# Kernel optimization log

Hardware: AMD Instinct MI355X
Metric: run time of the kernel (lower is better)

The kernel has to match this reference:

```python
import jax, jax.numpy as jnp
import numpy as np

# uniform-measure init scales from torch_model.init_embedding_scale()
MIN_MEAN = (0.0001 + 0.01) / 2.0
MIN_VAR = 0.01 - MIN_MEAN
DELTA_MEAN = (0.9 + 0.999) / 2.0
DELTA_VAR = 0.999 - DELTA_MEAN
EPS = 1e-8

B, V, D = 131072, 100000, 128


def setup_inputs() -> dict:
    key = jax.random.key(0)
    k1, k2, k3, k4 = jax.random.split(key, 4)
    return {
        "t1x": jax.random.randint(k1, (B,), 0, V),
        "t2x": jax.random.randint(k2, (B,), 0, V),
        "min_embed_table": jax.random.normal(k3, (V, D), jnp.float32),
        "delta_embed_table": jax.random.normal(k4, (V, D), jnp.float32),
    }


def _log_vol(mn, mx):
    # log volume of a box under the uniform (unit-cube) measure; [*, D] -> [*]
    return jnp.sum(jnp.log(jnp.maximum(mx - mn, EPS)), axis=-1)


def _box(idx, min_table, delta_table):
    # embedding lookup + affine rescale into the unit cube (get_word_embedding)
    mn = min_table[idx] * MIN_VAR + MIN_MEAN
    dl = delta_table[idx] * DELTA_VAR + DELTA_MEAN
    return mn, mn + dl


def reference(t1x, t2x, min_embed_table, delta_embed_table):
    t1_min, t1_max = _box(t1x, min_embed_table, delta_embed_table)  # [B, D]
    t2_min, t2_max = _box(t2x, min_embed_table, delta_embed_table)

    # unit_cube.calc_join_and_meet
    join_min = jnp.minimum(t1_min, t2_min)
    join_max = jnp.maximum(t1_max, t2_max)
    meet_min = jnp.maximum(t1_min, t2_min)
    meet_max = jnp.minimum(t1_max, t2_max)
    disjoint = jnp.any(meet_max <= meet_min, axis=-1)  # [B] bool

    t1_log = _log_vol(t1_min, t1_max)      # [B]
    t2_log = _log_vol(t2_min, t2_max)
    meet_log = _log_vol(meet_min, meet_max)
    join_log = _log_vol(join_min, join_max)

    # log P(t1 | t2) = log vol(meet) - log vol(t2)
    cond_log = meet_log - t2_log

    # positive pairs: overlap -> -log P(t1|t2); disjoint -> upper-bound surrogate
    # upper bound: P(t1, t2) <= vol(t1)*vol(t2)/vol(join)  =>  P(t1|t2) <= vol(t1)/vol(join)
    pos_overlap = -cond_log
    pos_disjoint = -(t1_log - join_log)

    # negative pairs: overlap -> -log(1 - P(t1|t2)); disjoint -> 0 loss
    neg_overlap = -jnp.log(jnp.maximum(1.0 - jnp.exp(cond_log), EPS))

    # vectorized version of the per-sample python loop over the disjoint flag
    train_pos_prob = jnp.where(disjoint, pos_disjoint, pos_overlap)  # [B]
    train_neg_prob = jnp.where(disjoint, jnp.zeros_like(neg_overlap), neg_overlap)
    return train_pos_prob, train_neg_prob
```

## Files before the change

kernel.cpp:

```cpp
#include <hip/hip_runtime.h>
#include <math.h>


#define EPSF 1e-8f

__global__ __launch_bounds__(256) void box_loss_kernel(
    const int* __restrict__ t1x, const int* __restrict__ t2x,
    const float* __restrict__ min_t, const float* __restrict__ delta_t,
    float* __restrict__ out, int B)
{
    const float MIN_MEAN   = (float)((0.0001 + 0.01) / 2.0);
    const float MIN_VAR    = (float)(0.01 - (0.0001 + 0.01) / 2.0);
    const float DELTA_MEAN = (float)((0.9 + 0.999) / 2.0);
    const float DELTA_VAR  = (float)(0.999 - (0.9 + 0.999) / 2.0);

    int gid  = blockIdx.x * blockDim.x + threadIdx.x;
    int s    = gid >> 5;
    int lane = threadIdx.x & 31;
    if (s >= B) return;

    long i1 = (long)t1x[s];
    long i2 = (long)t2x[s];

    const float4* m1 = reinterpret_cast<const float4*>(min_t   + i1 * 128);
    const float4* d1 = reinterpret_cast<const float4*>(delta_t + i1 * 128);
    const float4* m2 = reinterpret_cast<const float4*>(min_t   + i2 * 128);
    const float4* d2 = reinterpret_cast<const float4*>(delta_t + i2 * 128);

    float4 vm1 = m1[lane];
    float4 vd1 = d1[lane];
    float4 vm2 = m2[lane];
    float4 vd2 = d2[lane];

    const float* pm1 = reinterpret_cast<const float*>(&vm1);
    const float* pd1 = reinterpret_cast<const float*>(&vd1);
    const float* pm2 = reinterpret_cast<const float*>(&vm2);
    const float* pd2 = reinterpret_cast<const float*>(&vd2);

    float t1_log = 0.f, t2_log = 0.f, meet_log = 0.f, join_log = 0.f;
    int disjoint = 0;

    #pragma unroll
    for (int k = 0; k < 4; ++k) {
        float t1min = fmaf(pm1[k], MIN_VAR, MIN_MEAN);
        float t1dl  = fmaf(pd1[k], DELTA_VAR, DELTA_MEAN);
        float t1max = t1min + t1dl;

        float t2min = fmaf(pm2[k], MIN_VAR, MIN_MEAN);
        float t2dl  = fmaf(pd2[k], DELTA_VAR, DELTA_MEAN);
        float t2max = t2min + t2dl;

        float jm = fminf(t1min, t2min);
        float jM = fmaxf(t1max, t2max);
        float mm = fmaxf(t1min, t2min);
        float mM = fminf(t1max, t2max);

        disjoint |= (mM <= mm) ? 1 : 0;

        t1_log   += __logf(fmaxf(t1max - t1min, EPSF));
        t2_log   += __logf(fmaxf(t2max - t2min, EPSF));
        meet_log += __logf(fmaxf(mM - mm, EPSF));
        join_log += __logf(fmaxf(jM - jm, EPSF));
    }

    #pragma unroll
    for (int m = 16; m >= 1; m >>= 1) {
        t1_log   += __shfl_xor(t1_log,   m, 64);
        t2_log   += __shfl_xor(t2_log,   m, 64);
        meet_log += __shfl_xor(meet_log, m, 64);
        join_log += __shfl_xor(join_log, m, 64);
        disjoint |= __shfl_xor(disjoint, m, 64);
    }

    if (lane == 0) {
        float cond = meet_log - t2_log;
        float pos, neg;
        if (disjoint) {
            pos = join_log - t1_log;
            neg = 0.f;
        } else {
            pos = -cond;
            neg = -logf(fmaxf(1.f - expf(cond), EPSF));
        }
        out[s]     = pos;
        out[B + s] = neg;
    }
}

extern "C" void kernel_launch(void* const* d_in, const int* in_sizes, int n_in,
                              void* d_out, int out_size, void* d_ws, size_t ws_size,
                              hipStream_t stream) {
    const int*   t1x     = (const int*)d_in[0];
    const int*   t2x     = (const int*)d_in[1];
    const float* min_t   = (const float*)d_in[2];
    const float* delta_t = (const float*)d_in[3];
    float*       out     = (float*)d_out;

    int B = in_sizes[0];
    int threads = 256;
    int blocks  = (B * 32 + threads - 1) / threads;
    box_loss_kernel<<<blocks, threads, 0, stream>>>(t1x, t2x, min_t, delta_t, out, B);
}
```

Baseline: 141.2 us.

## Use 8 lanes per sample and replace per-element logs with products

Each sample is now handled by 8 lanes instead of 32, with every lane loading four float4 chunks per row. Per-element logarithms are replaced by running products of the widths, followed by one log per accumulator. The disjoint flag now comes from the minimum meet width. This cuts transcendental work, shuffle rounds and redundant index loads. Products of 16 widths could underflow when meet widths are near EPS (1e-8), which risks precision.

Result: faster. 137.4 us (-2.7%).

```diff
diff --git a/kernel.cpp b/kernel.cpp
--- a/kernel.cpp
+++ b/kernel.cpp
@@ -15,68 +15,81 @@
     const float DELTA_VAR  = (float)(0.999 - (0.9 + 0.999) / 2.0);
 
     int gid  = blockIdx.x * blockDim.x + threadIdx.x;
-    int s    = gid >> 5;
-    int lane = threadIdx.x & 31;
+    int s    = gid >> 3;
+    int lane = threadIdx.x & 7;
     if (s >= B) return;
 
-    long i1 = (long)t1x[s];
-    long i2 = (long)t2x[s];
+    size_t i1 = (size_t)t1x[s];
+    size_t i2 = (size_t)t2x[s];
 
     const float4* m1 = reinterpret_cast<const float4*>(min_t   + i1 * 128);
     const float4* d1 = reinterpret_cast<const float4*>(delta_t + i1 * 128);
     const float4* m2 = reinterpret_cast<const float4*>(min_t   + i2 * 128);
     const float4* d2 = reinterpret_cast<const float4*>(delta_t + i2 * 128);
 
-    float4 vm1 = m1[lane];
-    float4 vd1 = d1[lane];
-    float4 vm2 = m2[lane];
-    float4 vd2 = d2[lane];
+    float4 a1[4], b1[4], a2[4], b2[4];
+    #pragma unroll
+    for (int c = 0; c < 4; ++c) {
+        int off = c * 8 + lane;
+        a1[c] = m1[off];
+        b1[c] = d1[off];
+        a2[c] = m2[off];
+        b2[c] = d2[off];
+    }
 
-    const float* pm1 = reinterpret_cast<const float*>(&vm1);
-    const float* pd1 = reinterpret_cast<const float*>(&vd1);
-    const float* pm2 = reinterpret_cast<const float*>(&vm2);
-    const float* pd2 = reinterpret_cast<const float*>(&vd2);
-
-    float t1_log = 0.f, t2_log = 0.f, meet_log = 0.f, join_log = 0.f;
-    int disjoint = 0;
+    float p1 = 1.f, p2 = 1.f, pm = 1.f, pj = 1.f;
+    float wmin = 1e30f;
 
     #pragma unroll
-    for (int k = 0; k < 4; ++k) {
-        float t1min = fmaf(pm1[k], MIN_VAR, MIN_MEAN);
-        float t1dl  = fmaf(pd1[k], DELTA_VAR, DELTA_MEAN);
-        float t1max = t1min + t1dl;
+    for (int c = 0; c < 4; ++c) {
+        const float* pa1 = reinterpret_cast<const float*>(&a1[c]);
+        const float* pb1 = reinterpret_cast<const float*>(&b1[c]);
+        const float* pa2 = reinterpret_cast<const float*>(&a2[c]);
+        const float* pb2 = reinterpret_cast<const float*>(&b2[c]);
+        #pragma unroll
+        for (int k = 0; k < 4; ++k) {
+            float t1min = fmaf(pa1[k], MIN_VAR, MIN_MEAN);
+            float w1    = fmaf(pb1[k], DELTA_VAR, DELTA_MEAN);
+            float t2min = fmaf(pa2[k], MIN_VAR, MIN_MEAN);
+            float w2    = fmaf(pb2[k], DELTA_VAR, DELTA_MEAN);
+            float t1max = t1min + w1;
+            float t2max = t2min + w2;
 
-        float t2min = fmaf(pm2[k], MIN_VAR, MIN_MEAN);
-        float t2dl  = fmaf(pd2[k], DELTA_VAR, DELTA_MEAN);
-        float t2max = t2min + t2dl;
+            float mm_ = fmaxf(t1min, t2min);
+            float mM_ = fminf(t1max, t2max);
+            float jm_ = fminf(t1min, t2min);
+            float jM_ = fmaxf(t1max, t2max);
 
-        float jm = fminf(t1min, t2min);
-        float jM = fmaxf(t1max, t2max);
-        float mm = fmaxf(t1min, t2min);
-        float mM = fminf(t1max, t2max);
+            float wm = mM_ - mm_;
+            float wj = jM_ - jm_;
 
-        disjoint |= (mM <= mm) ? 1 : 0;
-
-        t1_log   += __logf(fmaxf(t1max - t1min, EPSF));
-        t2_log   += __logf(fmaxf(t2max - t2min, EPSF));
-        meet_log += __logf(fmaxf(mM - mm, EPSF));
-        join_log += __logf(fmaxf(jM - jm, EPSF));
+            wmin = fminf(wmin, wm);
+            p1 *= w1;
+            p2 *= w2;
+            pm *= fmaxf(wm, EPSF);
+            pj *= wj;
+        }
     }
 
+    float l1 = __logf(p1);
+    float l2 = __logf(p2);
+    float lm = __logf(pm);
+    float lj = __logf(pj);
+
     #pragma unroll
-    for (int m = 16; m >= 1; m >>= 1) {
-        t1_log   += __shfl_xor(t1_log,   m, 64);
-        t2_log   += __shfl_xor(t2_log,   m, 64);
-        meet_log += __shfl_xor(meet_log, m, 64);
-        join_log += __shfl_xor(join_log, m, 64);
-        disjoint |= __shfl_xor(disjoint, m, 64);
+    for (int m = 4; m >= 1; m >>= 1) {
+        l1   += __shfl_xor(l1,   m, 64);
+        l2   += __shfl_xor(l2,   m, 64);
+        lm   += __shfl_xor(lm,   m, 64);
+        lj   += __shfl_xor(lj,   m, 64);
+        wmin  = fminf(wmin, __shfl_xor(wmin, m, 64));
     }
 
     if (lane == 0) {
-        float cond = meet_log - t2_log;
+        float cond = lm - l2;
         float pos, neg;
-        if (disjoint) {
-            pos = join_log - t1_log;
+        if (wmin <= 0.f) {
+            pos = lj - l1;
             neg = 0.f;
         } else {
             pos = -cond;
@@ -98,6 +111,6 @@
 
     int B = in_sizes[0];
     int threads = 256;
-    int blocks  = (B * 32 + threads - 1) / threads;
+    int blocks  = (B * 8 + threads - 1) / threads;
     box_loss_kernel<<<blocks, threads, 0, stream>>>(t1x, t2x, min_t, delta_t, out, B);
 }
```
